# Optimization experiments

Measured on AMD Instinct MI355X. Metric: run time of the kernel, lower is better.

Reference implementation:

```python
import jax, jax.numpy as jnp
import numpy as np

B = 16384      # batch size
NL = 131072    # total labels (~8 per image)
S = 7          # grid size
NCLS = 20


def setup_inputs() -> dict:
    key = jax.random.key(0)
    k1, k2, k3, k4, k5 = jax.random.split(key, 5)
    # predictions in [0,1): slices 24:26 / 28:30 feed sqrt(x+1e-6)
    output = jax.random.uniform(k1, (B, S, S, 30), dtype=jnp.float32)
    bidx = jax.random.randint(k2, (NL,), 0, B).astype(jnp.float32)
    cls = jax.random.randint(k3, (NL,), 0, NCLS).astype(jnp.float32)
    cxy = jax.random.uniform(k4, (NL, 2), minval=0.01, maxval=0.99, dtype=jnp.float32)
    wh = jax.random.uniform(k5, (NL, 2), minval=0.05, maxval=0.5, dtype=jnp.float32)
    labels = jnp.concatenate([bidx[:, None], cls[:, None], cxy, wh], axis=1)
    return {"output": output, "labels": labels}


def _iou(a, g):
    # center-format boxes [n,4] = (cx, cy, w, h), standard IoU
    ax1, ax2 = a[:, 0] - a[:, 2] / 2, a[:, 0] + a[:, 2] / 2
    ay1, ay2 = a[:, 1] - a[:, 3] / 2, a[:, 1] + a[:, 3] / 2
    gx1, gx2 = g[:, 0] - g[:, 2] / 2, g[:, 0] + g[:, 2] / 2
    gy1, gy2 = g[:, 1] - g[:, 3] / 2, g[:, 1] + g[:, 3] / 2
    iw = jnp.maximum(0.0, jnp.minimum(ax2, gx2) - jnp.maximum(ax1, gx1))
    ih = jnp.maximum(0.0, jnp.minimum(ay2, gy2) - jnp.maximum(ay1, gy1))
    inter = iw * ih
    union = a[:, 2] * a[:, 3] + g[:, 2] * g[:, 3] - inter
    return inter / (union + 1e-6)


def reference(output, labels):
    w_coord, w_noobj, eps = 5.0, 0.5, 1e-6
    bsz = output.shape[0]
    # no-object confidence penalty over ALL cells (per-label responsible-box
    # terms subtract their share back below, exactly as the torch loop does)
    noobj_loss = w_noobj * jnp.sum(output[..., 20] ** 2 + output[..., 21] ** 2)

    b = labels[:, 0].astype(jnp.int32)
    c = labels[:, 1].astype(jnp.int32)
    gt = labels[:, 2:6]                       # global (cx, cy, w, h)
    rowf = jnp.floor(gt[:, 0] * S)            # int(cx*7)
    colf = jnp.floor(gt[:, 1] * S)            # int(cy*7)
    row = rowf.astype(jnp.int32)
    col = colf.astype(jnp.int32)

    p = output[b, row, col]                   # [nl, 30] gather of responsible cells

    # classification loss
    onehot = jax.nn.one_hot(c, NCLS, dtype=p.dtype)
    class_loss = jnp.sum((p[:, :NCLS] - onehot) ** 2)

    # predicted boxes in global normalized coords: (row + bx)/7 (img_size cancels)
    def to_global(box):
        return jnp.stack(
            [(rowf + box[:, 0]) / S, (colf + box[:, 1]) / S, box[:, 2], box[:, 3]],
            axis=1,
        )

    iou1 = _iou(to_global(p[:, 22:26]), gt)
    iou2 = _iou(to_global(p[:, 26:30]), gt)
    use1 = iou1 >= iou2

    # gt center relative to its cell: gt*7 - row (img_size cancels)
    gt_cell_xy = jnp.stack([gt[:, 0] * S - rowf, gt[:, 1] * S - colf], axis=1)

    xy = jnp.where(use1[:, None], p[:, 22:24], p[:, 26:28])
    wh = jnp.where(use1[:, None], p[:, 24:26], p[:, 28:30])
    coor_loss = w_coord * (
        jnp.sum((xy - gt_cell_xy) ** 2)
        + jnp.sum((jnp.sqrt(wh + eps) - jnp.sqrt(gt[:, 2:4] + eps)) ** 2)
    )

    conf_pred = jnp.where(use1, p[:, 20], p[:, 21])
    conf_tgt = jnp.where(use1, iou1, iou2)
    conf_loss = noobj_loss + jnp.sum(
        (conf_pred - conf_tgt) ** 2 - w_noobj * conf_pred ** 2
    )

    return (coor_loss + conf_loss + class_loss) / bsz
```

## Files before the change

kernel.cpp:

```cpp
#include <hip/hip_runtime.h>
#include <math.h>

constexpr int   kS    = 7;
constexpr int   kNCls = 20;
constexpr int   kB    = 16384;
constexpr float kWCoord = 5.0f;
constexpr float kWNoobj = 0.5f;
constexpr float kEps    = 1e-6f;

__device__ __forceinline__ void block_reduce_atomic(float v, float* acc) {
    #pragma unroll
    for (int off = 32; off > 0; off >>= 1)
        v += __shfl_down(v, off, 64);
    __shared__ float smem[4];
    const int lane = threadIdx.x & 63;
    const int wv   = threadIdx.x >> 6;
    if (lane == 0) smem[wv] = v;
    __syncthreads();
    if (threadIdx.x == 0) {
        float t = smem[0] + smem[1] + smem[2] + smem[3];
        atomicAdd(acc, t);
    }
}

__global__ void __launch_bounds__(256) noobj_kernel(const float4* __restrict__ o4,
                                                    int n4,
                                                    float* __restrict__ acc) {
    float sum = 0.0f;
    const int stride = gridDim.x * blockDim.x;
    for (int i = blockIdx.x * blockDim.x + threadIdx.x; i < n4; i += stride) {
        float4 v = o4[i];
        int ch0 = (i * 4) % 30;
        float vv[4] = {v.x, v.y, v.z, v.w};
        #pragma unroll
        for (int j = 0; j < 4; ++j) {
            int ch = ch0 + j;
            ch = (ch >= 30) ? (ch - 30) : ch;
            const bool hit = (ch == 20) || (ch == 21);
            const float x = vv[j];
            sum += hit ? x * x : 0.0f;
        }
    }
    sum *= kWNoobj;
    block_reduce_atomic(sum, acc);
}

__device__ __forceinline__ float iou_f(float ax, float ay, float aw, float ah,
                                       float gx, float gy, float gw, float gh) {
    const float ax1 = ax - aw * 0.5f, ax2 = ax + aw * 0.5f;
    const float ay1 = ay - ah * 0.5f, ay2 = ay + ah * 0.5f;
    const float gx1 = gx - gw * 0.5f, gx2 = gx + gw * 0.5f;
    const float gy1 = gy - gh * 0.5f, gy2 = gy + gh * 0.5f;
    const float iw = fmaxf(0.0f, fminf(ax2, gx2) - fmaxf(ax1, gx1));
    const float ih = fmaxf(0.0f, fminf(ay2, gy2) - fmaxf(ay1, gy1));
    const float inter = iw * ih;
    const float uni = aw * ah + gw * gh - inter;
    return inter / (uni + kEps);
}

__global__ void __launch_bounds__(256) label_kernel(const float* __restrict__ out,
                                                    const float* __restrict__ labels,
                                                    int nl,
                                                    float* __restrict__ acc) {
    const int l = blockIdx.x * blockDim.x + threadIdx.x;
    float sum = 0.0f;
    if (l < nl) {
        const float2* lab2 = reinterpret_cast<const float2*>(labels + (size_t)l * 6);
        const float2 l0 = lab2[0];
        const float2 l1 = lab2[1];
        const float2 l2 = lab2[2];
        const int   b  = (int)l0.x;
        const int   c  = (int)l0.y;
        const float gx = l1.x, gy = l1.y, gw = l2.x, gh = l2.y;

        const float rowf = floorf(gx * (float)kS);
        const float colf = floorf(gy * (float)kS);
        const int row = (int)rowf;
        const int col = (int)colf;

        const float* p = out + ((size_t)b * (kS * kS) + row * kS + col) * 30;
        const float2* p2 = reinterpret_cast<const float2*>(p);
        float pv[30];
        #pragma unroll
        for (int j = 0; j < 15; ++j) {
            const float2 t = p2[j];
            pv[2 * j]     = t.x;
            pv[2 * j + 1] = t.y;
        }

        float cl = 0.0f;
        #pragma unroll
        for (int j = 0; j < kNCls; ++j) {
            const float d = pv[j] - ((j == c) ? 1.0f : 0.0f);
            cl += d * d;
        }

        const float inv_s = 1.0f / (float)kS;
        const float b1x = (rowf + pv[22]) * inv_s;
        const float b1y = (colf + pv[23]) * inv_s;
        const float b2x = (rowf + pv[26]) * inv_s;
        const float b2y = (colf + pv[27]) * inv_s;
        const float g1x = (rowf + pv[22]) / (float)kS;
        const float g1y = (colf + pv[23]) / (float)kS;
        const float g2x = (rowf + pv[26]) / (float)kS;
        const float g2y = (colf + pv[27]) / (float)kS;
        (void)b1x; (void)b1y; (void)b2x; (void)b2y;

        const float iou1 = iou_f(g1x, g1y, pv[24], pv[25], gx, gy, gw, gh);
        const float iou2 = iou_f(g2x, g2y, pv[28], pv[29], gx, gy, gw, gh);
        const bool use1 = (iou1 >= iou2);

        const float gtx_cell = gx * (float)kS - rowf;
        const float gty_cell = gy * (float)kS - colf;
        const float px = use1 ? pv[22] : pv[26];
        const float py = use1 ? pv[23] : pv[27];
        const float pw = use1 ? pv[24] : pv[28];
        const float ph = use1 ? pv[25] : pv[29];
        const float dx = px - gtx_cell;
        const float dy = py - gty_cell;
        const float dw = sqrtf(pw + kEps) - sqrtf(gw + kEps);
        const float dh = sqrtf(ph + kEps) - sqrtf(gh + kEps);
        const float coord = kWCoord * (dx * dx + dy * dy + dw * dw + dh * dh);

        const float cp = use1 ? pv[20] : pv[21];
        const float ct = use1 ? iou1 : iou2;
        const float conf = (cp - ct) * (cp - ct) - kWNoobj * cp * cp;

        sum = cl + coord + conf;
    }
    block_reduce_atomic(sum, acc);
}

__global__ void finalize_kernel(const float* __restrict__ acc, float* __restrict__ out) {
    out[0] = acc[0] * (1.0f / (float)kB);
}

extern "C" void kernel_launch(void* const* d_in, const int* in_sizes, int n_in,
                              void* d_out, int out_size, void* d_ws, size_t ws_size,
                              hipStream_t stream) {
    const float* output = (const float*)d_in[0];
    const float* labels = (const float*)d_in[1];
    float* out = (float*)d_out;
    float* acc = (float*)d_ws;

    const int n_out_elems = in_sizes[0];
    const int n4 = n_out_elems / 4;
    const int nl = in_sizes[1] / 6;

    hipMemsetAsync(acc, 0, sizeof(float), stream);

    const int blocks1 = 2048;
    noobj_kernel<<<blocks1, 256, 0, stream>>>((const float4*)output, n4, acc);

    const int blocks2 = (nl + 255) / 256;
    label_kernel<<<blocks2, 256, 0, stream>>>(output, labels, nl, acc);

    finalize_kernel<<<1, 1, 0, stream>>>(acc, out);
}
```

Before: 171.2 us.

## Fuse noobj and label passes, load only conf channels, drop atomics

Merges the no-object sum and the per-label loss into one grid-stride kernel. The no-object pass now reads only channels 20-21 of each cell as a float2 instead of streaming the whole tensor with float4 loads. Per-block partials are written to the workspace and reduced in a finalize kernel, which removes the memset and the global atomics. The strided 8-byte reads at a 120-byte pitch may still pull in most cache lines, so the bytes saved depend on sector granularity.

```diff
diff --git a/kernel.cpp b/kernel.cpp
--- a/kernel.cpp
+++ b/kernel.cpp
@@ -1,48 +1,32 @@
 #include <hip/hip_runtime.h>
 #include <math.h>
 
-constexpr int   kS    = 7;
-constexpr int   kNCls = 20;
-constexpr int   kB    = 16384;
+constexpr int   kS      = 7;
+constexpr int   kNCls   = 20;
+constexpr int   kB      = 16384;
+constexpr int   kNCells = kB * kS * kS;
 constexpr float kWCoord = 5.0f;
 constexpr float kWNoobj = 0.5f;
 constexpr float kEps    = 1e-6f;
 
-__device__ __forceinline__ void block_reduce_atomic(float v, float* acc) {
+constexpr int kBlocks = 2048;
+constexpr int kThreads = 256;
+
+__device__ __forceinline__ float block_reduce(float v) {
     #pragma unroll
     for (int off = 32; off > 0; off >>= 1)
         v += __shfl_down(v, off, 64);
-    __shared__ float smem[4];
+    __shared__ float smem[kThreads / 64];
     const int lane = threadIdx.x & 63;
     const int wv   = threadIdx.x >> 6;
     if (lane == 0) smem[wv] = v;
     __syncthreads();
+    float t = 0.0f;
     if (threadIdx.x == 0) {
-        float t = smem[0] + smem[1] + smem[2] + smem[3];
-        atomicAdd(acc, t);
+        #pragma unroll
+        for (int i = 0; i < kThreads / 64; ++i) t += smem[i];
     }
-}
-
-__global__ void __launch_bounds__(256) noobj_kernel(const float4* __restrict__ o4,
-                                                    int n4,
-                                                    float* __restrict__ acc) {
-    float sum = 0.0f;
-    const int stride = gridDim.x * blockDim.x;
-    for (int i = blockIdx.x * blockDim.x + threadIdx.x; i < n4; i += stride) {
-        float4 v = o4[i];
-        int ch0 = (i * 4) % 30;
-        float vv[4] = {v.x, v.y, v.z, v.w};
-        #pragma unroll
-        for (int j = 0; j < 4; ++j) {
-            int ch = ch0 + j;
-            ch = (ch >= 30) ? (ch - 30) : ch;
-            const bool hit = (ch == 20) || (ch == 21);
-            const float x = vv[j];
-            sum += hit ? x * x : 0.0f;
-        }
-    }
-    sum *= kWNoobj;
-    block_reduce_atomic(sum, acc);
+    return t;
 }
 
 __device__ __forceinline__ float iou_f(float ax, float ay, float aw, float ah,
@@ -58,18 +42,25 @@
     return inter / (uni + kEps);
 }
 
-__global__ void __launch_bounds__(256) label_kernel(const float* __restrict__ out,
-                                                    const float* __restrict__ labels,
-                                                    int nl,
-                                                    float* __restrict__ acc) {
-    const int l = blockIdx.x * blockDim.x + threadIdx.x;
+__global__ void __launch_bounds__(kThreads)
+fused_kernel(const float* __restrict__ out,
+             const float* __restrict__ labels,
+             int nl,
+             float* __restrict__ partials) {
+    const int tid    = blockIdx.x * blockDim.x + threadIdx.x;
+    const int stride = gridDim.x * blockDim.x;
     float sum = 0.0f;
-    if (l < nl) {
+
+    for (int c = tid; c < kNCells; c += stride) {
+        const float2 v = *reinterpret_cast<const float2*>(out + (size_t)c * 30 + 20);
+        sum += kWNoobj * (v.x * v.x + v.y * v.y);
+    }
+
+    for (int l = tid; l < nl; l += stride) {
         const float2* lab2 = reinterpret_cast<const float2*>(labels + (size_t)l * 6);
         const float2 l0 = lab2[0];
         const float2 l1 = lab2[1];
         const float2 l2 = lab2[2];
-        const int   b  = (int)l0.x;
         const int   c  = (int)l0.y;
         const float gx = l1.x, gy = l1.y, gw = l2.x, gh = l2.y;
 
@@ -77,6 +68,7 @@
         const float colf = floorf(gy * (float)kS);
         const int row = (int)rowf;
         const int col = (int)colf;
+        const int b   = (int)l0.x;
 
         const float* p = out + ((size_t)b * (kS * kS) + row * kS + col) * 30;
         const float2* p2 = reinterpret_cast<const float2*>(p);
@@ -95,16 +87,10 @@
             cl += d * d;
         }
 
-        const float inv_s = 1.0f / (float)kS;
-        const float b1x = (rowf + pv[22]) * inv_s;
-        const float b1y = (colf + pv[23]) * inv_s;
-        const float b2x = (rowf + pv[26]) * inv_s;
-        const float b2y = (colf + pv[27]) * inv_s;
         const float g1x = (rowf + pv[22]) / (float)kS;
         const float g1y = (colf + pv[23]) / (float)kS;
         const float g2x = (rowf + pv[26]) / (float)kS;
         const float g2y = (colf + pv[27]) / (float)kS;
-        (void)b1x; (void)b1y; (void)b2x; (void)b2y;
 
         const float iou1 = iou_f(g1x, g1y, pv[24], pv[25], gx, gy, gw, gh);
         const float iou2 = iou_f(g2x, g2y, pv[28], pv[29], gx, gy, gw, gh);
@@ -126,13 +112,19 @@
         const float ct = use1 ? iou1 : iou2;
         const float conf = (cp - ct) * (cp - ct) - kWNoobj * cp * cp;
 
-        sum = cl + coord + conf;
+        sum += cl + coord + conf;
     }
-    block_reduce_atomic(sum, acc);
+
+    const float bsum = block_reduce(sum);
+    if (threadIdx.x == 0) partials[blockIdx.x] = bsum;
 }
 
-__global__ void finalize_kernel(const float* __restrict__ acc, float* __restrict__ out) {
-    out[0] = acc[0] * (1.0f / (float)kB);
+__global__ void __launch_bounds__(kThreads)
+finalize_kernel(const float* __restrict__ partials, int n, float* __restrict__ out) {
+    float s = 0.0f;
+    for (int i = threadIdx.x; i < n; i += blockDim.x) s += partials[i];
+    const float t = block_reduce(s);
+    if (threadIdx.x == 0) out[0] = t * (1.0f / (float)kB);
 }
 
 extern "C" void kernel_launch(void* const* d_in, const int* in_sizes, int n_in,
@@ -141,19 +133,10 @@
     const float* output = (const float*)d_in[0];
     const float* labels = (const float*)d_in[1];
     float* out = (float*)d_out;
-    float* acc = (float*)d_ws;
+    float* partials = (float*)d_ws;
 
-    const int n_out_elems = in_sizes[0];
-    const int n4 = n_out_elems / 4;
     const int nl = in_sizes[1] / 6;
 
-    hipMemsetAsync(acc, 0, sizeof(float), stream);
-
-    const int blocks1 = 2048;
-    noobj_kernel<<<blocks1, 256, 0, stream>>>((const float4*)output, n4, acc);
-
-    const int blocks2 = (nl + 255) / 256;
-    label_kernel<<<blocks2, 256, 0, stream>>>(output, labels, nl, acc);
-
-    finalize_kernel<<<1, 1, 0, stream>>>(acc, out);
+    fused_kernel<<<kBlocks, kThreads, 0, stream>>>(output, labels, nl, partials);
+    finalize_kernel<<<1, kThreads, 0, stream>>>(partials, kBlocks, out);
 }
```

New measurement: 146.3 us. 14.6% less time.
